# Kernel optimization log

Measured on AMD Instinct MI355X. Metric: run time of the kernel, lower is better.

Reference implementation:

```python
import jax, jax.numpy as jnp
import numpy as np

P = 3
N_DIGITS = 4
MAX_IDX = 63  # module clamps indices with min(idx, 63)
EPS = 1e-10


def _padic_table(p=P, n_digits=N_DIGITS):
    n = p ** n_digits  # 81
    d = np.abs(np.arange(n)[:, None] - np.arange(n)[None, :])
    val = np.zeros((n, n), dtype=np.int64)
    tmp = d.copy()
    # valuation: count factors of p (at most ~n_digits*log levels; 8 iters is plenty for n=81)
    for _ in range(8):
        div = (tmp > 0) & (tmp % p == 0)
        val += div
        tmp = np.where(div, tmp // p, tmp)
    dist = np.where(d > 0, float(p) ** (-val.astype(np.float64)), 0.0)
    return jnp.asarray(dist, dtype=jnp.float32)


def setup_inputs() -> dict:
    key = jax.random.key(0)
    k1, k2 = jax.random.split(key)
    codon_embeddings = jax.random.normal(k1, (8, 1024, 256), dtype=jnp.float32)
    codon_indices = jax.random.randint(k2, (8, 1024), 0, 64)
    padic_distances = _padic_table()
    return {
        "codon_embeddings": codon_embeddings,
        "codon_indices": codon_indices,
        "padic_distances": padic_distances,
    }


def reference(codon_embeddings, codon_indices, padic_distances):
    B, S, D = codon_embeddings.shape
    x = codon_embeddings.reshape(-1, D)  # (N, D), N = B*S

    # Euclidean cdist (p=2): d2 = |xi|^2 + |xj|^2 - 2 xi.xj
    sq = jnp.sum(x * x, axis=-1)
    d2 = sq[:, None] + sq[None, :] - 2.0 * (x @ x.T)
    d2 = jnp.maximum(d2, 0.0)
    # safe sqrt (zero diag -> zero distance, no nan grads)
    emb_dist = jnp.where(d2 > 0, jnp.sqrt(jnp.where(d2 > 0, d2, 1.0)), 0.0)

    # vectorized equivalent of the python double-loop gather
    idx = jnp.minimum(codon_indices.reshape(-1), MAX_IDX)  # (N,)
    target_dist = padic_distances[idx][:, idx]  # (N, N)

    emb_n = emb_dist / (jnp.max(emb_dist) + EPS)
    tgt_n = target_dist / (jnp.max(target_dist) + EPS)

    e = emb_n.reshape(-1) - jnp.mean(emb_n)
    t = tgt_n.reshape(-1) - jnp.mean(tgt_n)
    corr = jnp.sum(e * t) / (jnp.sqrt(jnp.sum(e * e) * jnp.sum(t * t)) + EPS)
    return 1.0 - corr
```

## Files before the change

### kernel.cpp

```cpp
#include <hip/hip_runtime.h>
#include <math.h>

typedef __attribute__((ext_vector_type(8))) short short8;
typedef __attribute__((ext_vector_type(16))) float f32x16;

#if defined(__has_builtin)
#if __has_builtin(__builtin_amdgcn_global_load_lds)
#define HAVE_GLL 1
#endif
#if __has_builtin(__builtin_amdgcn_sqrtf)
#define FSQRT(x) __builtin_amdgcn_sqrtf(x)
#endif
#endif
#ifndef HAVE_GLL
#define HAVE_GLL 0
#endif
#ifndef FSQRT
#define FSQRT(x) sqrtf(x)
#endif

__device__ __forceinline__ unsigned short f2bf(float f) {
    unsigned int x = __float_as_uint(f);
    unsigned int r = (x + 0x7fffu + ((x >> 16) & 1u)) >> 16;
    return (unsigned short)r;
}

__device__ __forceinline__ unsigned char f2e4m3(float f) {
    unsigned u = __float_as_uint(f);
    unsigned s = (u >> 24) & 0x80u;
    float a = fabsf(f);
    if (a < 0.015625f) return (unsigned char)s;
    if (a > 448.f)     return (unsigned char)(s | 0x7E);
    unsigned au = u & 0x7FFFFFFFu;
    unsigned mlo = au & 0xFFFFFu;
    unsigned keep = au >> 20;
    keep += (mlo > 0x80000u) || (mlo == 0x80000u && (keep & 1u));
    int e = (int)(keep >> 3) - 127;
    unsigned m3 = keep & 7u;
    if (e < -6) return (unsigned char)s;
    if (e > 8)  return (unsigned char)(s | 0x7E);
    return (unsigned char)(s | (unsigned)((e + 7) << 3) | m3);
}
__device__ __forceinline__ float e4m3dec(unsigned char c) {
    if (!(c & 0x7F)) return 0.f;
    unsigned s = ((unsigned)(c & 0x80)) << 24;
    unsigned e = (c >> 3) & 0xF;
    unsigned m = c & 7u;
    return __uint_as_float(s | ((e - 7 + 127) << 23) | (m << 20));
}


__global__ void rowstats_kernel(const float* __restrict__ x, const int* __restrict__ idx,
                                float* __restrict__ sq, int* __restrict__ ci,
                                unsigned char* __restrict__ x8,
                                int N, int D, int doCvt) {
    int wave0 = (blockIdx.x * blockDim.x + threadIdx.x) >> 6;
    int lane  = threadIdx.x & 63;
    int nw    = (gridDim.x * blockDim.x) >> 6;
    for (int row = wave0; row < N; row += nw) {
        const float* rp = x + (size_t)row * D;
        float s = 0.f;
        for (int c = lane * 4; c < D; c += 256) {
            float4 v = *reinterpret_cast<const float4*>(rp + c);
            if (doCvt) {
                uchar4 h;
                h.x = f2e4m3(v.x); h.y = f2e4m3(v.y); h.z = f2e4m3(v.z); h.w = f2e4m3(v.w);
                *reinterpret_cast<uchar4*>(x8 + (size_t)row * D + c) = h;
                float q0 = e4m3dec(h.x), q1 = e4m3dec(h.y), q2 = e4m3dec(h.z), q3 = e4m3dec(h.w);
                s = fmaf(q0, q0, s); s = fmaf(q1, q1, s);
                s = fmaf(q2, q2, s); s = fmaf(q3, q3, s);
            } else {
                s = fmaf(v.x, v.x, s); s = fmaf(v.y, v.y, s);
                s = fmaf(v.z, v.z, s); s = fmaf(v.w, v.w, s);
            }
        }
        #pragma unroll
        for (int o = 32; o > 0; o >>= 1) s += __shfl_down(s, o, 64);
        if (lane == 0) {
            sq[row] = s;
            int v = idx[row]; if (v > 63) v = 63;
            ci[row] = v;
        }
    }
}

__device__ __forceinline__ void tri_decode(int L, int NB, int chunks, int doSwz, int& bi, int& bj) {
    if (doSwz) { int xcd = L & 7, pos = L >> 3; L = xcd * chunks + pos; }
    float disc = (float)((2 * NB + 1) * (2 * NB + 1) - 8 * L);
    int b = (int)(((float)(2 * NB + 1) - sqrtf(disc)) * 0.5f);
    if (b < 0) b = 0; if (b > NB - 1) b = NB - 1;
    while (b + 1 <= NB - 1 && ((b + 1) * NB - ((b + 1) * b) / 2) <= L) ++b;
    while (b > 0 && (b * NB - (b * (b - 1)) / 2) > L) --b;
    bi = b; bj = b + (L - (b * NB - (b * (b - 1)) / 2));
}

template<bool DIAG>
__device__ __forceinline__ void epilogueQ(const f32x16 (&acc)[2][2],
                                          const float* sqA, const float* sqB,
                                          const int* caA, const int* cbB, const float* tbl,
                                          float* red, int w, int lane, int wr, int wc,
                                          double* partials, int pidx) {
    const int l31 = lane & 31;
    const int hi4 = (lane >> 5) << 2;
    float sb[2]; int cb[2];
    #pragma unroll
    for (int ni = 0; ni < 2; ++ni) {
        int c = wc * 64 + ni * 32 + l31;
        sb[ni] = sqB[c]; cb[ni] = cbB[c];
    }
    float se = 0.f, sd2 = 0.f, setv = 0.f;
    #pragma unroll
    for (int mi = 0; mi < 2; ++mi)
        #pragma unroll
        for (int r = 0; r < 16; ++r) {
            int rr = wr * 64 + mi * 32 + (r & 3) + ((r >> 2) << 3) + hi4;
            float sa_ = sqA[rr]; int ca_ = caA[rr];
            #pragma unroll
            for (int ni = 0; ni < 2; ++ni) {
                float d2 = fmaf(-2.f, acc[mi][ni][r], sa_ + sb[ni]);
                d2 = fmaxf(d2, 0.f);
                if (DIAG) { if (rr == wc * 64 + ni * 32 + l31) d2 = 0.f; }
                float e = FSQRT(d2);
                int delta = ca_ - cb[ni]; if (delta < 0) delta = -delta;
                float t = tbl[delta];
                se += e; sd2 += d2; setv = fmaf(e, t, setv);
            }
        }
    #pragma unroll
    for (int o = 32; o > 0; o >>= 1) {
        se  += __shfl_down(se, o, 64);
        sd2 += __shfl_down(sd2, o, 64);
        setv += __shfl_down(setv, o, 64);
    }
    if (lane == 0) { red[w * 3 + 0] = se; red[w * 3 + 1] = sd2; red[w * 3 + 2] = setv; }
    __syncthreads();
    if (w == 0 && lane == 0) {
        double wgt = DIAG ? 1.0 : 2.0;
        double S0 = 0, S1 = 0, S2 = 0;
        #pragma unroll
        for (int i = 0; i < 4; ++i) {
            S0 += (double)red[i * 3 + 0]; S1 += (double)red[i * 3 + 1]; S2 += (double)red[i * 3 + 2];
        }
        double* p = partials + (size_t)pidx * 4;
        p[0] = wgt * S0; p[1] = wgt * S1; p[2] = wgt * S2;
    }
}

__global__ __launch_bounds__(256, 4) void pair128f8_kernel(
        const unsigned char* __restrict__ x8, const float* __restrict__ table,
        const float* __restrict__ sq, const int* __restrict__ ci,
        int NB, int chunks, int doSwz, double* __restrict__ partials) {
#if HAVE_GLL
    constexpr int D = 256;
    __shared__ char lds[16384];
    __shared__ float sqA[128], sqB[128], tbl[64];
    __shared__ int   caA[128], cbB[128];
    __shared__ float red[12];

    int bi, bj;
    tri_decode(blockIdx.x, NB, chunks, doSwz, bi, bj);

    const int tid = threadIdx.x;
    const int w = tid >> 6, lane = tid & 63;
    const int wr = w >> 1, wc = w & 1;
    const int l31 = lane & 31, khalf = lane >> 5;

    if (tid < 64) tbl[tid] = table[tid];
    if (tid < 128) { sqA[tid] = sq[bi * 128 + tid]; caA[tid] = ci[bi * 128 + tid]; }
    else { int t2 = tid - 128; sqB[t2] = sq[bj * 128 + t2]; cbB[t2] = ci[bj * 128 + t2]; }

    const int prow0 = ((w >= 2) ? bj : bi) * 128;
    auto STAGE4 = [&](int t) {
        #pragma unroll
        for (int q = 0; q < 4; ++q) {
            int u   = (w << 2) + q;
            int blk = (u >> 1) & 3;
            int kh  = u & 1;
            const unsigned char* g = x8 + (size_t)(prow0 + blk * 32 + (lane >> 1)) * D
                                        + t * 64 + kh * 32 + (lane & 1) * 16;
            char* dst = lds + (u << 10);
            __builtin_amdgcn_global_load_lds(
                (__attribute__((address_space(1))) void*)(void*)g,
                (__attribute__((address_space(3))) void*)dst, 16, 0, 0);
        }
    };

    f32x16 acc[2][2];
    #pragma unroll
    for (int a = 0; a < 2; ++a)
        #pragma unroll
        for (int b = 0; b < 2; ++b)
            #pragma unroll
            for (int r = 0; r < 16; ++r) acc[a][b][r] = 0.f;

    for (int t = 0; t < 4; ++t) {
        STAGE4(t);
        asm volatile("s_waitcnt vmcnt(0)" ::: "memory");
        __builtin_amdgcn_s_barrier();
        const int foff = l31 * 32 + khalf * 8;
        #pragma unroll
        for (int kh = 0; kh < 2; ++kh) {
            #pragma unroll
            for (int s = 0; s < 2; ++s) {
                long a_[2], b_[2];
                #pragma unroll
                for (int mi = 0; mi < 2; ++mi)
                    a_[mi] = *reinterpret_cast<const long*>(lds + (((((wr << 1) + mi) << 1) + kh) << 10) + s * 16 + foff);
                #pragma unroll
                for (int ni = 0; ni < 2; ++ni)
                    b_[ni] = *reinterpret_cast<const long*>(lds + ((8 + (((wc << 1) + ni) << 1) + kh) << 10) + s * 16 + foff);
                #pragma unroll
                for (int mi = 0; mi < 2; ++mi)
                    #pragma unroll
                    for (int ni = 0; ni < 2; ++ni)
                        acc[mi][ni] = __builtin_amdgcn_mfma_f32_32x32x16_fp8_fp8(a_[mi], b_[ni], acc[mi][ni], 0, 0, 0);
            }
        }
        __builtin_amdgcn_s_barrier();
    }

    if (bi == bj) epilogueQ<true >(acc, sqA, sqB, caA, cbB, tbl, red, w, lane, wr, wc, partials, blockIdx.x);
    else          epilogueQ<false>(acc, sqA, sqB, caA, cbB, tbl, red, w, lane, wr, wc, partials, blockIdx.x);
#endif
}

__global__ void pair_fb_kernel(const float* __restrict__ x, const float* __restrict__ table,
                               const float* __restrict__ sq, const int* __restrict__ ci,
                               int D, int NB, int chunks, int doSwz,
                               double* __restrict__ partials) {
    typedef __attribute__((ext_vector_type(4))) float f32x4v;
    int bi, bj;
    tri_decode(blockIdx.x, NB, chunks, doSwz, bi, bj);

    __shared__ float sqA[128], sqB[128], tbl[64];
    __shared__ int   caA[128], cbB[128];
    __shared__ float red[12];

    const int tid = threadIdx.x;
    const int w = tid >> 6, lane = tid & 63;
    const int wr = w >> 1, wc = w & 1;
    const int l15 = lane & 15, koct = lane >> 4;

    if (tid < 64) tbl[tid] = table[tid];
    if (tid < 128) { sqA[tid] = sq[bi * 128 + tid]; caA[tid] = ci[bi * 128 + tid]; }
    else { int t2 = tid - 128; sqB[t2] = sq[bj * 128 + t2]; cbB[t2] = ci[bj * 128 + t2]; }
    __syncthreads();

    f32x4v acc[4][4];
    #pragma unroll
    for (int a = 0; a < 4; ++a)
        #pragma unroll
        for (int b = 0; b < 4; ++b) acc[a][b] = (f32x4v){0.f, 0.f, 0.f, 0.f};

    const float* pa = x + (size_t)(bi * 128 + wr * 64 + l15) * D + koct * 8;
    const float* pb = x + (size_t)(bj * 128 + wc * 64 + l15) * D + koct * 8;
    const size_t rs = (size_t)16 * D;
    for (int k = 0; k < D; k += 32) {
        short8 af[4], bfv[4];
        #pragma unroll
        for (int m = 0; m < 4; ++m) {
            float4 f0 = *reinterpret_cast<const float4*>(pa + m * rs + k);
            float4 f1 = *reinterpret_cast<const float4*>(pa + m * rs + k + 4);
            short8 v;
            v[0]=(short)f2bf(f0.x); v[1]=(short)f2bf(f0.y); v[2]=(short)f2bf(f0.z); v[3]=(short)f2bf(f0.w);
            v[4]=(short)f2bf(f1.x); v[5]=(short)f2bf(f1.y); v[6]=(short)f2bf(f1.z); v[7]=(short)f2bf(f1.w);
            af[m] = v;
        }
        #pragma unroll
        for (int n = 0; n < 4; ++n) {
            float4 f0 = *reinterpret_cast<const float4*>(pb + n * rs + k);
            float4 f1 = *reinterpret_cast<const float4*>(pb + n * rs + k + 4);
            short8 v;
            v[0]=(short)f2bf(f0.x); v[1]=(short)f2bf(f0.y); v[2]=(short)f2bf(f0.z); v[3]=(short)f2bf(f0.w);
            v[4]=(short)f2bf(f1.x); v[5]=(short)f2bf(f1.y); v[6]=(short)f2bf(f1.z); v[7]=(short)f2bf(f1.w);
            bfv[n] = v;
        }
        #pragma unroll
        for (int fm = 0; fm < 4; ++fm)
            #pragma unroll
            for (int fn = 0; fn < 4; ++fn)
                acc[fm][fn] = __builtin_amdgcn_mfma_f32_16x16x32_bf16(af[fm], bfv[fn], acc[fm][fn], 0, 0, 0);
    }

    const int rsub = koct << 2;
    float sb[4]; int cb[4];
    #pragma unroll
    for (int fn = 0; fn < 4; ++fn) {
        int c = wc * 64 + fn * 16 + l15;
        sb[fn] = sqB[c]; cb[fn] = cbB[c];
    }
    float se = 0.f, sd2 = 0.f, setv = 0.f;
    const bool diag = (bi == bj);
    #pragma unroll
    for (int fm = 0; fm < 4; ++fm)
        #pragma unroll
        for (int rg = 0; rg < 4; ++rg) {
            int r = wr * 64 + fm * 16 + rsub + rg;
            float sa_ = sqA[r]; int ca_ = caA[r];
            #pragma unroll
            for (int fn = 0; fn < 4; ++fn) {
                float d2 = fmaf(-2.f, acc[fm][fn][rg], sa_ + sb[fn]);
                d2 = fmaxf(d2, 0.f);
                if (diag && r == wc * 64 + fn * 16 + l15) d2 = 0.f;
                float e = FSQRT(d2);
                int delta = ca_ - cb[fn]; if (delta < 0) delta = -delta;
                float t = tbl[delta];
                se += e; sd2 += d2; setv = fmaf(e, t, setv);
            }
        }
    #pragma unroll
    for (int o = 32; o > 0; o >>= 1) {
        se  += __shfl_down(se, o, 64);
        sd2 += __shfl_down(sd2, o, 64);
        setv += __shfl_down(setv, o, 64);
    }
    if (lane == 0) { red[w * 3 + 0] = se; red[w * 3 + 1] = sd2; red[w * 3 + 2] = setv; }
    __syncthreads();
    if (tid == 0) {
        double wgt = diag ? 1.0 : 2.0;
        double S0 = 0, S1 = 0, S2 = 0;
        #pragma unroll
        for (int i = 0; i < 4; ++i) {
            S0 += (double)red[i * 3 + 0]; S1 += (double)red[i * 3 + 1]; S2 += (double)red[i * 3 + 2];
        }
        double* p = partials + (size_t)blockIdx.x * 4;
        p[0] = wgt * S0; p[1] = wgt * S1; p[2] = wgt * S2;
    }
}

__global__ void finalize_kernel(const double* __restrict__ partials, int nL,
                                const int* __restrict__ civ, int N,
                                const float* __restrict__ table, int tdim,
                                float* __restrict__ out) {
    __shared__ unsigned int h[64];
    __shared__ double red[4][5];
    const int tid = threadIdx.x;
    if (tid < 64) h[tid] = 0u;
    __syncthreads();
    for (int i = tid; i < N; i += 256) atomicAdd(&h[civ[i]], 1u);
    __syncthreads();

    double se = 0, sd2 = 0, setv = 0;
    for (int i = tid; i < nL; i += 256) {
        const double* p = partials + (size_t)i * 4;
        se += p[0]; sd2 += p[1]; setv += p[2];
    }
    double st = 0, stt = 0;
    for (int c = tid; c < 4096; c += 256) {
        int u = c >> 6, v = c & 63;
        double t = (double)table[u * tdim + v];
        double hh = (double)h[u] * (double)h[v];
        st += hh * t; stt += hh * t * t;
    }
    #pragma unroll
    for (int o = 32; o > 0; o >>= 1) {
        se += __shfl_down(se, o, 64);
        sd2 += __shfl_down(sd2, o, 64);
        setv += __shfl_down(setv, o, 64);
        st += __shfl_down(st, o, 64);
        stt += __shfl_down(stt, o, 64);
    }
    int w = tid >> 6;
    if ((tid & 63) == 0) { red[w][0] = se; red[w][1] = sd2; red[w][2] = setv; red[w][3] = st; red[w][4] = stt; }
    __syncthreads();
    if (tid == 0) {
        double S[5] = {0, 0, 0, 0, 0};
        #pragma unroll
        for (int i = 0; i < 4; ++i)
            #pragma unroll
            for (int q = 0; q < 5; ++q) S[q] += red[i][q];
        double nn = (double)N * (double)N;
        double cet = S[2] - S[0] * S[3] / nn;
        double cee = S[1] - S[0] * S[0] / nn;
        double ctt = S[4] - S[3] * S[3] / nn;
        double corr = cet / (sqrt(cee * ctt) + 1e-10);
        out[0] = (float)(1.0 - corr);
    }
}

extern "C" void kernel_launch(void* const* d_in, const int* in_sizes, int n_in,
                              void* d_out, int out_size, void* d_ws, size_t ws_size,
                              hipStream_t stream) {
    const float* x     = (const float*)d_in[0];
    const int*   idx   = (const int*)d_in[1];
    const float* table = (const float*)d_in[2];

    const int N = in_sizes[1];
    const int D = in_sizes[0] / N;
    int tdim = 1;
    while (tdim * tdim < in_sizes[2]) ++tdim;

    char* ws = (char*)d_ws;
    double*        partials = (double*)(ws + 512);
    float*         sqv      = (float*)(ws + 67584);
    int*           civ      = (int*)(ws + 67584 + (size_t)N * 4);
    unsigned char* x8       = (unsigned char*)(ws + 67584 + (size_t)N * 8);

    size_t need = 67584 + (size_t)N * 8 + (size_t)N * D;
    const bool f8 = (ws_size >= need) && (D == 256) && (N % 128 == 0);

    rowstats_kernel<<<dim3(1024), 256, 0, stream>>>(x, idx, sqv, civ, x8, N, D, f8 ? 1 : 0);

    const int NB = N / 128;
    const int nL = NB * (NB + 1) / 2;
    const int doSwz = (nL % 8 == 0) ? 1 : 0;
    const int chunks = nL / 8;

    if (f8)
        pair128f8_kernel<<<dim3(nL), 256, 0, stream>>>(x8, table, sqv, civ, NB, chunks, doSwz, partials);
    else
        pair_fb_kernel<<<dim3(nL), 256, 0, stream>>>(x, table, sqv, civ, D, NB, chunks, doSwz, partials);

    finalize_kernel<<<1, 256, 0, stream>>>(partials, nL, civ, N, table, tdim, (float*)d_out);
}
```

Baseline: 51.85 us.

## Swizzle LDS staging layout to avoid bank conflicts; use hardware fp8 conversion

The global-to-LDS staging now permutes which row and half each lane writes, and the MFMA fragment reads use a matching rotated position, so the 8-byte LDS reads across a wave no longer collide on the same banks. Separately, the row-stats kernel uses the hardware packed fp8 convert and decode builtins when available, replacing the software e4m3 rounding routine. The swizzle adds a little index arithmetic. The hardware conversion may differ from the software rounding in saturation and denormal handling.

```diff
diff --git a/kernel.cpp b/kernel.cpp
--- a/kernel.cpp
+++ b/kernel.cpp
@@ -11,12 +11,18 @@
 #if __has_builtin(__builtin_amdgcn_sqrtf)
 #define FSQRT(x) __builtin_amdgcn_sqrtf(x)
 #endif
+#if __has_builtin(__builtin_amdgcn_cvt_pk_fp8_f32) && __has_builtin(__builtin_amdgcn_cvt_f32_fp8)
+#define HAVE_CVT8 1
+#endif
 #endif
 #ifndef HAVE_GLL
 #define HAVE_GLL 0
 #endif
 #ifndef FSQRT
 #define FSQRT(x) sqrtf(x)
+#endif
+#ifndef HAVE_CVT8
+#define HAVE_CVT8 0
 #endif
 
 __device__ __forceinline__ unsigned short f2bf(float f) {
@@ -63,10 +69,21 @@
         for (int c = lane * 4; c < D; c += 256) {
             float4 v = *reinterpret_cast<const float4*>(rp + c);
             if (doCvt) {
+#if HAVE_CVT8
+                unsigned pk = 0;
+                pk = (unsigned)__builtin_amdgcn_cvt_pk_fp8_f32(v.x, v.y, (int)pk, false);
+                pk = (unsigned)__builtin_amdgcn_cvt_pk_fp8_f32(v.z, v.w, (int)pk, true);
+                *reinterpret_cast<unsigned*>(x8 + (size_t)row * D + c) = pk;
+                float q0 = __builtin_amdgcn_cvt_f32_fp8((int)pk, 0);
+                float q1 = __builtin_amdgcn_cvt_f32_fp8((int)pk, 1);
+                float q2 = __builtin_amdgcn_cvt_f32_fp8((int)pk, 2);
+                float q3 = __builtin_amdgcn_cvt_f32_fp8((int)pk, 3);
+#else
                 uchar4 h;
                 h.x = f2e4m3(v.x); h.y = f2e4m3(v.y); h.z = f2e4m3(v.z); h.w = f2e4m3(v.w);
                 *reinterpret_cast<uchar4*>(x8 + (size_t)row * D + c) = h;
                 float q0 = e4m3dec(h.x), q1 = e4m3dec(h.y), q2 = e4m3dec(h.z), q3 = e4m3dec(h.w);
+#endif
                 s = fmaf(q0, q0, s); s = fmaf(q1, q1, s);
                 s = fmaf(q2, q2, s); s = fmaf(q3, q3, s);
             } else {
@@ -169,6 +186,11 @@
     if (tid < 128) { sqA[tid] = sq[bi * 128 + tid]; caA[tid] = ci[bi * 128 + tid]; }
     else { int t2 = tid - 128; sqB[t2] = sq[bj * 128 + t2]; cbB[t2] = ci[bj * 128 + t2]; }
 
+    const int pa_ = lane >> 3;
+    const int pt  = ((lane & 7) - pa_) & 7;
+    const int srow = pa_ * 4 + (pt >> 1);
+    const int sh   = pt & 1;
+
     const int prow0 = ((w >= 2) ? bj : bi) * 128;
     auto STAGE4 = [&](int t) {
         #pragma unroll
@@ -176,8 +198,8 @@
             int u   = (w << 2) + q;
             int blk = (u >> 1) & 3;
             int kh  = u & 1;
-            const unsigned char* g = x8 + (size_t)(prow0 + blk * 32 + (lane >> 1)) * D
-                                        + t * 64 + kh * 32 + (lane & 1) * 16;
+            const unsigned char* g = x8 + (size_t)(prow0 + blk * 32 + srow) * D
+                                        + t * 64 + kh * 32 + sh * 16;
             char* dst = lds + (u << 10);
             __builtin_amdgcn_global_load_lds(
                 (__attribute__((address_space(1))) void*)(void*)g,
@@ -185,6 +207,10 @@
         }
     };
 
+    const int ra = l31 >> 2, rb = l31 & 3;
+    const int pos0 = ra * 8 + ((2 * rb + 0 + ra) & 7);
+    const int pos1 = ra * 8 + ((2 * rb + 1 + ra) & 7);
+
     f32x16 acc[2][2];
     #pragma unroll
     for (int a = 0; a < 2; ++a)
@@ -197,18 +223,18 @@
         STAGE4(t);
         asm volatile("s_waitcnt vmcnt(0)" ::: "memory");
         __builtin_amdgcn_s_barrier();
-        const int foff = l31 * 32 + khalf * 8;
         #pragma unroll
         for (int kh = 0; kh < 2; ++kh) {
             #pragma unroll
             for (int s = 0; s < 2; ++s) {
+                const int fo = (s ? pos1 : pos0) * 16 + khalf * 8;
                 long a_[2], b_[2];
                 #pragma unroll
                 for (int mi = 0; mi < 2; ++mi)
-                    a_[mi] = *reinterpret_cast<const long*>(lds + (((((wr << 1) + mi) << 1) + kh) << 10) + s * 16 + foff);
+                    a_[mi] = *reinterpret_cast<const long*>(lds + (((((wr << 1) + mi) << 1) + kh) << 10) + fo);
                 #pragma unroll
                 for (int ni = 0; ni < 2; ++ni)
-                    b_[ni] = *reinterpret_cast<const long*>(lds + ((8 + (((wc << 1) + ni) << 1) + kh) << 10) + s * 16 + foff);
+                    b_[ni] = *reinterpret_cast<const long*>(lds + ((8 + (((wc << 1) + ni) << 1) + kh) << 10) + fo);
                 #pragma unroll
                 for (int mi = 0; mi < 2; ++mi)
                     #pragma unroll
```

Measured after the change: 45.47 us (median of 3 runs). -12.3%, faster.
